# Kernel tuning notes

Measured on AMD Instinct MI355X. Metric: run time of the kernel, lower is better.

Reference implementation:

```python
import jax, jax.numpy as jnp
import numpy as np


def setup_inputs() -> dict:
    key = jax.random.key(0)
    ks = jax.random.split(key, 8)
    vocab, d_word, d_topic = 100000, 300, 256
    N, L = 16384, 8  # num spans, max span length (padded ragged layout)
    V = jax.random.normal(ks[0], (vocab, d_word), jnp.float32)
    k_w = jax.random.normal(ks[1], (d_topic, d_word), jnp.float32) * (1.0 / np.sqrt(d_word))
    k_b = jnp.zeros((d_topic,), jnp.float32)
    q_w = jax.random.normal(ks[2], (d_topic, d_topic), jnp.float32) * (1.0 / np.sqrt(d_topic))
    q_b = jnp.zeros((d_topic,), jnp.float32)
    topic_emb = jax.random.normal(ks[3], (d_topic,), jnp.float32)
    verb_ids = jax.random.randint(ks[4], (N, L), 0, vocab)
    span_len = jax.random.randint(ks[5], (N,), 1, L + 1)  # at least 1 valid token per span
    return {"topic_emb": topic_emb, "verb_ids": verb_ids, "span_len": span_len,
            "V": V, "k_w": k_w, "k_b": k_b, "q_w": q_w, "q_b": q_b}


def reference(topic_emb, verb_ids, span_len, V, k_w, k_b, q_w, q_b):
    # Batched version of the per-span Python loop:
    # value = Embedding(verb)            -> [N, L, d_word]
    # key   = Linear_k(value)            -> [N, L, d_topic]
    # query = Linear_q(topic_emb)        -> [d_topic] (same for every span)
    # out_i = SDPA(query, key_i, value_i)-> [d_word]
    d_topic = q_w.shape[0]
    value = V[verb_ids]                                   # [N, L, d_word] gather
    keyp = jnp.einsum('nld,td->nlt', value, k_w) + k_b    # [N, L, d_topic]
    query = q_w @ topic_emb + q_b                         # [d_topic]
    scores = jnp.einsum('nlt,t->nl', keyp, query) / jnp.sqrt(jnp.float32(d_topic))
    # mask padded positions (ragged spans) with -inf before softmax
    valid = jnp.arange(value.shape[1])[None, :] < span_len[:, None]
    scores = jnp.where(valid, scores, -jnp.inf)
    attn = jax.nn.softmax(scores, axis=-1)                # [N, L]
    return jnp.einsum('nl,nld->nd', attn, value)          # [N, d_word]
```

## Files before the change

kernel.cpp:

```cpp
#include <hip/hip_runtime.h>
#include <hip/hip_bf16.h>
#include <math.h>


#define SPAN_L 8
#define DW 300
#define DT 256
#define Q_OFF 320

typedef float f32x4 __attribute__((ext_vector_type(4)));

__device__ __forceinline__ float wave_reduce(float p) {
    #pragma unroll
    for (int m = 1; m < 64; m <<= 1) p += __shfl_xor(p, m, 64);
    return p;
}

__global__ __launch_bounds__(256) void tva_prep_q(
    const float* __restrict__ topic_emb,
    const float* __restrict__ q_w,
    const float* __restrict__ q_b,
    float* __restrict__ wc)
{
    const int wave = threadIdx.x >> 6;
    const int lane = threadIdx.x & 63;
    const float4 te4 = ((const float4*)topic_emb)[lane];
    const int gw = blockIdx.x * 4 + wave;
    #pragma unroll
    for (int j = 0; j < 2; ++j) {
        const int r = gw * 2 + j;
        const float4 qr = ((const float4*)(q_w + r * DT))[lane];
        float p = qr.x * te4.x + qr.y * te4.y + qr.z * te4.z + qr.w * te4.w;
        p = wave_reduce(p);
        if (lane == 0) wc[Q_OFF + r] = p + q_b[r];
    }
}

__global__ __launch_bounds__(256) void tva_prep_w(
    const float* __restrict__ k_w,
    const float* __restrict__ k_b,
    float* __restrict__ wc)
{
    __shared__ float part[4][4];
    const int b = blockIdx.x;
    const int tid = threadIdx.x;
    const int wave = tid >> 6;
    const int lane = tid & 63;

    if (b == 75) {
        if (wave == 0) {
            float p = 0.f;
            #pragma unroll
            for (int j = 0; j < 4; ++j) {
                const int t = lane + 64 * j;
                p += k_b[t] * wc[Q_OFF + t];
            }
            p = wave_reduce(p);
            if (lane == 0) wc[DW] = p * 0.0625f;
        }
        return;
    }

    const int d_off = tid & 3;
    const int t0 = tid >> 2;
    const int d = 4 * b + d_off;
    float p = 0.f;
    #pragma unroll
    for (int j = 0; j < 4; ++j) {
        const int t = t0 + 64 * j;
        p += k_w[t * DW + d] * wc[Q_OFF + t];
    }
    #pragma unroll
    for (int m = 4; m < 64; m <<= 1) p += __shfl_xor(p, m, 64);
    if (lane < 4) part[wave][lane] = p;
    __syncthreads();
    if (tid < 4)
        wc[4 * b + tid] = (part[0][tid] + part[1][tid] + part[2][tid] + part[3][tid]) * 0.0625f;
}

__global__ __launch_bounds__(256, 4) void tva_main(
    const float* __restrict__ V,
    const int*   __restrict__ verb_ids,
    const int*   __restrict__ span_len,
    const float* __restrict__ wc,
    float* __restrict__ out,
    int N)
{
    const int wave = threadIdx.x >> 6;
    const int lane = threadIdx.x & 63;
    const int n = blockIdx.x * 4 + wave;
    if (n >= N) return;

    const bool tail = (lane < 11);
    const float4* w4 = (const float4*)wc;
    const float4 wv0 = w4[lane];
    const float4 wv1 = tail ? w4[64 + lane] : make_float4(0.f, 0.f, 0.f, 0.f);
    const float  c   = wc[DW];

    const int len = span_len[n];

    const int4* ids4 = (const int4*)(verb_ids + n * SPAN_L);
    const int4 ia = ids4[0];
    const int4 ib = ids4[1];
    int rows[SPAN_L] = {ia.x, ia.y, ia.z, ia.w, ib.x, ib.y, ib.z, ib.w};

    float4 v0[SPAN_L], v1[SPAN_L];
    #pragma unroll
    for (int l = 0; l < SPAN_L; ++l) {
        if (l < len) {
            const float4* vr = (const float4*)(V + (long)rows[l] * DW);
            v0[l] = vr[lane];
            v1[l] = tail ? vr[64 + lane] : make_float4(0.f, 0.f, 0.f, 0.f);
        } else {
            v0[l] = make_float4(0.f, 0.f, 0.f, 0.f);
            v1[l] = make_float4(0.f, 0.f, 0.f, 0.f);
        }
    }

    float s[SPAN_L];
    #pragma unroll
    for (int l = 0; l < SPAN_L; ++l) {
        float p = v0[l].x * wv0.x + v0[l].y * wv0.y + v0[l].z * wv0.z + v0[l].w * wv0.w
                + v1[l].x * wv1.x + v1[l].y * wv1.y + v1[l].z * wv1.z + v1[l].w * wv1.w;
        p = wave_reduce(p);
        s[l] = (l < len) ? (p + c) : -INFINITY;
    }

    float mx = s[0];
    #pragma unroll
    for (int l = 1; l < SPAN_L; ++l) mx = fmaxf(mx, s[l]);
    float e[SPAN_L];
    float denom = 0.f;
    #pragma unroll
    for (int l = 0; l < SPAN_L; ++l) { e[l] = __expf(s[l] - mx); denom += e[l]; }
    const float inv = 1.f / denom;

    f32x4 a0 = {0.f, 0.f, 0.f, 0.f};
    f32x4 a1 = {0.f, 0.f, 0.f, 0.f};
    #pragma unroll
    for (int l = 0; l < SPAN_L; ++l) {
        const float al = e[l] * inv;
        a0.x += al * v0[l].x; a0.y += al * v0[l].y; a0.z += al * v0[l].z; a0.w += al * v0[l].w;
        a1.x += al * v1[l].x; a1.y += al * v1[l].y; a1.z += al * v1[l].z; a1.w += al * v1[l].w;
    }

    f32x4* o4 = (f32x4*)(out + (long)n * DW);
    __builtin_nontemporal_store(a0, o4 + lane);
    if (tail) __builtin_nontemporal_store(a1, o4 + 64 + lane);
}

extern "C" void kernel_launch(void* const* d_in, const int* in_sizes, int n_in,
                              void* d_out, int out_size, void* d_ws, size_t ws_size,
                              hipStream_t stream) {
    const float* topic_emb = (const float*)d_in[0];
    const int*   verb_ids  = (const int*)  d_in[1];
    const int*   span_len  = (const int*)  d_in[2];
    const float* V         = (const float*)d_in[3];
    const float* k_w       = (const float*)d_in[4];
    const float* k_b       = (const float*)d_in[5];
    const float* q_w       = (const float*)d_in[6];
    const float* q_b       = (const float*)d_in[7];
    float* out = (float*)d_out;
    float* wc  = (float*)d_ws;

    const int N = in_sizes[2];

    tva_prep_q<<<32, 256, 0, stream>>>(topic_emb, q_w, q_b, wc);
    tva_prep_w<<<76, 256, 0, stream>>>(k_w, k_b, wc);
    tva_main<<<(N + 3) / 4, 256, 0, stream>>>(V, verb_ids, span_len, wc, out, N);
}
```

Before: 196.0 us.

## Fuse query and weight prep kernels into one launch; use 32-bit gather offsets

Result: slower. 206.9 us (+5.5%).

```diff
diff --git a/kernel.cpp b/kernel.cpp
--- a/kernel.cpp
+++ b/kernel.cpp
@@ -6,7 +6,7 @@
 #define SPAN_L 8
 #define DW 300
 #define DT 256
-#define Q_OFF 320
+#define PREP_WBLOCKS 19
 
 typedef float f32x4 __attribute__((ext_vector_type(4)));
 
@@ -16,44 +16,39 @@
     return p;
 }
 
-__global__ __launch_bounds__(256) void tva_prep_q(
+__global__ __launch_bounds__(1024) void tva_prep(
     const float* __restrict__ topic_emb,
     const float* __restrict__ q_w,
     const float* __restrict__ q_b,
-    float* __restrict__ wc)
-{
-    const int wave = threadIdx.x >> 6;
-    const int lane = threadIdx.x & 63;
-    const float4 te4 = ((const float4*)topic_emb)[lane];
-    const int gw = blockIdx.x * 4 + wave;
-    #pragma unroll
-    for (int j = 0; j < 2; ++j) {
-        const int r = gw * 2 + j;
-        const float4 qr = ((const float4*)(q_w + r * DT))[lane];
-        float p = qr.x * te4.x + qr.y * te4.y + qr.z * te4.z + qr.w * te4.w;
-        p = wave_reduce(p);
-        if (lane == 0) wc[Q_OFF + r] = p + q_b[r];
-    }
-}
-
-__global__ __launch_bounds__(256) void tva_prep_w(
     const float* __restrict__ k_w,
     const float* __restrict__ k_b,
     float* __restrict__ wc)
 {
-    __shared__ float part[4][4];
-    const int b = blockIdx.x;
-    const int tid = threadIdx.x;
+    __shared__ float q_lds[DT];
+    __shared__ float part[64][16];
+    const int tid  = threadIdx.x;
     const int wave = tid >> 6;
     const int lane = tid & 63;
 
-    if (b == 75) {
+    const float4 te4 = ((const float4*)topic_emb)[lane];
+    #pragma unroll 4
+    for (int i = 0; i < 16; ++i) {
+        const int r = wave * 16 + i;
+        const float4 qr = ((const float4*)(q_w + r * DT))[lane];
+        float p = qr.x * te4.x + qr.y * te4.y + qr.z * te4.z + qr.w * te4.w;
+        p = wave_reduce(p);
+        if (lane == 0) q_lds[r] = p + q_b[r];
+    }
+    __syncthreads();
+
+    const int b = blockIdx.x;
+    if (b == PREP_WBLOCKS) {
         if (wave == 0) {
             float p = 0.f;
             #pragma unroll
             for (int j = 0; j < 4; ++j) {
                 const int t = lane + 64 * j;
-                p += k_b[t] * wc[Q_OFF + t];
+                p += k_b[t] * q_lds[t];
             }
             p = wave_reduce(p);
             if (lane == 0) wc[DW] = p * 0.0625f;
@@ -61,21 +56,28 @@
         return;
     }
 
-    const int d_off = tid & 3;
-    const int t0 = tid >> 2;
-    const int d = 4 * b + d_off;
+    const int t0 = tid >> 4;
+    const int dj = tid & 15;
+    const int d  = b * 16 + dj;
     float p = 0.f;
-    #pragma unroll
-    for (int j = 0; j < 4; ++j) {
-        const int t = t0 + 64 * j;
-        p += k_w[t * DW + d] * wc[Q_OFF + t];
+    if (d < DW) {
+        #pragma unroll
+        for (int k = 0; k < 4; ++k) {
+            const int t = t0 + 64 * k;
+            p += k_w[t * DW + d] * q_lds[t];
+        }
     }
-    #pragma unroll
-    for (int m = 4; m < 64; m <<= 1) p += __shfl_xor(p, m, 64);
-    if (lane < 4) part[wave][lane] = p;
+    part[t0][dj] = p;
     __syncthreads();
-    if (tid < 4)
-        wc[4 * b + tid] = (part[0][tid] + part[1][tid] + part[2][tid] + part[3][tid]) * 0.0625f;
+    if (tid < 16) {
+        const int dd = b * 16 + tid;
+        if (dd < DW) {
+            float s = 0.f;
+            #pragma unroll
+            for (int k = 0; k < 64; ++k) s += part[k][tid];
+            wc[dd] = s * 0.0625f;
+        }
+    }
 }
 
 __global__ __launch_bounds__(256, 4) void tva_main(
@@ -104,13 +106,16 @@
     const int4 ib = ids4[1];
     int rows[SPAN_L] = {ia.x, ia.y, ia.z, ia.w, ib.x, ib.y, ib.z, ib.w};
 
+    const char* Vb = (const char*)V;
+    const uint32_t lane16 = (uint32_t)(lane * 16);
     float4 v0[SPAN_L], v1[SPAN_L];
     #pragma unroll
     for (int l = 0; l < SPAN_L; ++l) {
         if (l < len) {
-            const float4* vr = (const float4*)(V + (long)rows[l] * DW);
-            v0[l] = vr[lane];
-            v1[l] = tail ? vr[64 + lane] : make_float4(0.f, 0.f, 0.f, 0.f);
+            const uint32_t off = (uint32_t)rows[l] * (uint32_t)(DW * 4) + lane16;
+            v0[l] = *(const float4*)(Vb + off);
+            v1[l] = tail ? *(const float4*)(Vb + off + 1024u)
+                         : make_float4(0.f, 0.f, 0.f, 0.f);
         } else {
             v0[l] = make_float4(0.f, 0.f, 0.f, 0.f);
             v1[l] = make_float4(0.f, 0.f, 0.f, 0.f);
@@ -165,7 +170,6 @@
 
     const int N = in_sizes[2];
 
-    tva_prep_q<<<32, 256, 0, stream>>>(topic_emb, q_w, q_b, wc);
-    tva_prep_w<<<76, 256, 0, stream>>>(k_w, k_b, wc);
+    tva_prep<<<PREP_WBLOCKS + 1, 1024, 0, stream>>>(topic_emb, q_w, q_b, k_w, k_b, wc);
     tva_main<<<(N + 3) / 4, 256, 0, stream>>>(V, verb_ids, span_len, wc, out, N);
 }
```
